# Kernel optimization log

Hardware: AMD Instinct MI355X
Metric: run time of the kernel (lower is better)

## Reference

```python
import jax, jax.numpy as jnp
import numpy as np

B, V, N, IN_F, HEADS, OUT_F = 4, 4, 1000, 64, 4, 32
D = HEADS * OUT_F  # 128, concat=True
E = 64000
NEG_SLOPE = 0.2


def setup_inputs() -> dict:
    key = jax.random.key(0)
    ks = jax.random.split(key, 8)
    x = jax.random.normal(ks[0], (B, V, N, IN_F), jnp.float32)
    edge_index = jax.random.randint(ks[1], (2, E), 0, B * N, dtype=jnp.int64)
    W = jax.random.normal(ks[2], (HEADS * OUT_F, IN_F), jnp.float32) / np.sqrt(IN_F)
    att = jax.random.normal(ks[3], (1, HEADS, 2 * OUT_F), jnp.float32) * 0.1
    in_proj_w = jax.random.normal(ks[4], (3 * D, D), jnp.float32) / np.sqrt(D)
    in_proj_b = jnp.zeros((3 * D,), jnp.float32)
    out_proj_w = jax.random.normal(ks[5], (D, D), jnp.float32) / np.sqrt(D)
    out_proj_b = jnp.zeros((D,), jnp.float32)
    bias = jnp.zeros((D,), jnp.float32)
    return dict(x=x, W=W, att=att, in_proj_w=in_proj_w, in_proj_b=in_proj_b,
                out_proj_w=out_proj_w, out_proj_b=out_proj_b, bias=bias,
                edge_index=edge_index)


def reference(x, W, att, in_proj_w, in_proj_b, out_proj_w, out_proj_b, bias, edge_index):
    Bx, Vx, Nx, _ = x.shape
    Ntot = Bx * Nx
    # intra-view GAT: shared W across views
    h = jnp.einsum('bvni,oi->bvno', x, W).reshape(Bx, Vx, Nx, HEADS, OUT_F)
    # block-diagonal placement: h_full[b*V+v, b*N:(b+1)*N] = h[b,v]
    ib = jnp.arange(Bx)
    hf = jnp.zeros((Bx, Vx, Bx, Nx, HEADS, OUT_F), x.dtype).at[ib, :, ib].set(h)
    h_full = hf.reshape(Bx * Vx, Ntot, HEADS, OUT_F)
    # add self loops
    loops = jnp.arange(Ntot, dtype=edge_index.dtype)
    src = jnp.concatenate([edge_index[0], loops])
    dst = jnp.concatenate([edge_index[1], loops])
    # attention scores (faithful to source: flatten h_full over (B*V, Ntot) and
    # index with raw node ids, i.e. gathers from block 0 only)
    h_flat = h_full.reshape(Bx * Vx * Ntot, HEADS, OUT_F)
    h_cat = jnp.concatenate([h_flat[src], h_flat[dst]], axis=-1)  # [Etot, H, 2*OUT]
    att_in = jax.nn.leaky_relu(h_cat, NEG_SLOPE)
    scores = jnp.sum(att * att_in, axis=-1)  # [Etot, HEADS]
    # per-destination segment softmax
    seg_max = jax.ops.segment_max(scores, dst, num_segments=Ntot)
    seg_max = jax.lax.stop_gradient(jnp.where(jnp.isfinite(seg_max), seg_max, 0.0))
    ex = jnp.exp(scores - seg_max[dst])
    denom = jax.ops.segment_sum(ex, dst, num_segments=Ntot)
    alpha = ex / (denom[dst] + 1e-16)  # [Etot, HEADS]
    # scatter-add aggregation, broadcast over B*V rows
    msgs = h_full[:, src] * alpha[None, :, :, None]  # [B*V, Etot, H, OUT]
    out_full = jnp.zeros_like(h_full).at[:, dst].add(msgs)
    # extract each graph's own node block
    out = out_full.reshape(Bx, Vx, Bx, Nx, HEADS, OUT_F)[ib, :, ib]  # [B,V,N,H,OUT]
    h_gat = out.reshape(Bx, Vx, Nx, HEADS * OUT_F)  # concat heads
    # inter-view mixing: MHA over the V axis per node
    seq = h_gat.transpose(0, 2, 1, 3).reshape(Bx * Nx, Vx, D)
    q, k, v = jnp.split(seq @ in_proj_w.T + in_proj_b, 3, axis=-1)
    hd = D // HEADS
    sp = lambda t: t.reshape(Bx * Nx, Vx, HEADS, hd).transpose(0, 2, 1, 3)
    q, k, v = sp(q), sp(k), sp(v)
    aw = jax.nn.softmax(jnp.einsum('bhqd,bhkd->bhqk', q, k) / jnp.sqrt(jnp.asarray(hd, x.dtype)), axis=-1)
    ao = jnp.einsum('bhqk,bhkd->bhqd', aw, v).transpose(0, 2, 1, 3).reshape(Bx * Nx, Vx, D)
    mixed = ao @ out_proj_w.T + out_proj_b
    h_mixed = mixed.reshape(Bx, Nx, Vx, D).transpose(0, 2, 1, 3)  # [B,V,N,D]
    return h_mixed + bias
```

## Files before the change

### kernel.cpp

```cpp
#include <hip/hip_runtime.h>

#define NN 1000
#define HEADS_ 4
#define DM 128
#define EE 64000
#define NTOT 4000
#define ETOT 68000
#define CAP 48
#define EB 34
#define TB 10

__device__ void gemm64_k1(float* As, float* Bs, int mi, int ni,
                          const float* __restrict__ x, const float* __restrict__ W,
                          float* __restrict__ hbuf, const float* __restrict__ att,
                          float* __restrict__ ssrc, float* __restrict__ sdst) {
  int tid = threadIdx.x;
  int m0 = mi * 64, n0 = ni * 64;
  int tx = tid & 15, ty = tid >> 4;
  const float4* A4 = (const float4*)x;
  const float4* W4 = (const float4*)W;
  float acc[4][4] = {};

  __syncthreads();
  {
    int q = tid & 15, r0 = tid >> 4;
#pragma unroll
    for (int p = 0; p < 4; ++p) {
      int r = r0 + p * 16;
      float4 v = A4[(size_t)(m0 + r) * 16 + q];
      *(float4*)&As[r * 64 + ((q ^ ((r >> 2) & 15)) << 2)] = v;
    }
#pragma unroll
    for (int p = 0; p < 4; ++p) {
      int r = r0 + p * 16;
      float4 v = W4[(size_t)(n0 + r) * 16 + q];
      *(float4*)&Bs[r * 64 + ((q ^ ((r >> 2) & 15)) << 2)] = v;
    }
  }
  __syncthreads();
#pragma unroll 4
  for (int q = 0; q < 16; ++q) {
    float4 a[4], b[4];
    int sa = (q ^ ty) << 2;
    int sb = (q ^ tx) << 2;
#pragma unroll
    for (int i = 0; i < 4; ++i)
      a[i] = *(const float4*)&As[(ty * 4 + i) * 64 + sa];
#pragma unroll
    for (int j = 0; j < 4; ++j)
      b[j] = *(const float4*)&Bs[(tx * 4 + j) * 64 + sb];
#pragma unroll
    for (int i = 0; i < 4; ++i)
#pragma unroll
      for (int j = 0; j < 4; ++j)
        acc[i][j] += a[i].x * b[j].x + a[i].y * b[j].y
                   + a[i].z * b[j].z + a[i].w * b[j].w;
  }

  int nc = n0 + tx * 4;
#pragma unroll
  for (int i = 0; i < 4; ++i) {
    int m = m0 + ty * 4 + i;
    *(float4*)&hbuf[(size_t)m * DM + nc] =
        make_float4(acc[i][0], acc[i][1], acc[i][2], acc[i][3]);
  }

  if (m0 < NN) {
    int hsel = tx >> 3;
    int h = ni * 2 + hsel;
    int kb = (tx & 7) * 4;
    float a0[4], a1[4];
#pragma unroll
    for (int j = 0; j < 4; ++j) {
      a0[j] = att[h * 64 + kb + j];
      a1[j] = att[h * 64 + 32 + kb + j];
    }
#pragma unroll
    for (int i = 0; i < 4; ++i) {
      int m = m0 + ty * 4 + i;
      float p0 = 0.f, p1 = 0.f;
#pragma unroll
      for (int j = 0; j < 4; ++j) {
        float g = acc[i][j];
        float lr = g > 0.f ? g : 0.2f * g;
        p0 += a0[j] * lr;
        p1 += a1[j] * lr;
      }
      p0 += __shfl_xor(p0, 1, 16); p1 += __shfl_xor(p1, 1, 16);
      p0 += __shfl_xor(p0, 2, 16); p1 += __shfl_xor(p1, 2, 16);
      p0 += __shfl_xor(p0, 4, 16); p1 += __shfl_xor(p1, 4, 16);
      if ((tx & 7) == 0 && m < NN) {
        ssrc[m * HEADS_ + h] = p0;
        sdst[m * HEADS_ + h] = p1;
      }
    }
  }
}

__global__ __launch_bounds__(256) void k1_kernel(const float* __restrict__ x,
                                                 const float* __restrict__ W,
                                                 const float* __restrict__ att,
                                                 float* __restrict__ hbuf,
                                                 float* __restrict__ ssrc,
                                                 float* __restrict__ sdst,
                                                 const int* __restrict__ ei,
                                                 int* __restrict__ cnt,
                                                 int* __restrict__ elist,
                                                 const float* __restrict__ inw,
                                                 const float* __restrict__ outw,
                                                 float* __restrict__ inwT,
                                                 float* __restrict__ outwT) {
  __shared__ float smem[8192];
  int bid = blockIdx.x;
  if (bid < 500) {
    gemm64_k1(smem, smem + 4096, bid >> 1, bid & 1, x, W, hbuf, att, ssrc, sdst);
  } else if (bid < 500 + EB) {
    for (int e = (bid - 500) * 256 + threadIdx.x; e < ETOT; e += EB * 256) {
      int s, d;
      if (e < EE) { s = ei[e]; d = ei[EE + e]; }
      else { s = d = e - EE; }
      int pos = atomicAdd(&cnt[d], 1);
      if (pos < CAP) elist[d * CAP + pos] = s;
    }
  } else {
    int tb = bid - (500 + EB);
    if (tb < 8) {
      for (int g = tb * 6144 + threadIdx.x; g < (tb + 1) * 6144; g += 256) {
        int col = g >> 7, k = g & 127;
        inwT[k * 384 + col] = inw[(size_t)col * 128 + k];
      }
    } else {
      int ob = tb - 8;
      for (int g = ob * 8192 + threadIdx.x; g < (ob + 1) * 8192; g += 256) {
        int col = g >> 7, k = g & 127;
        outwT[k * 128 + col] = outw[(size_t)col * 128 + k];
      }
    }
  }
}

__global__ __launch_bounds__(256) void mega2_kernel(const int* __restrict__ cnt,
                                                    const int* __restrict__ elist,
                                                    const float* __restrict__ ssrc,
                                                    const float* __restrict__ sdst,
                                                    const float* __restrict__ hbuf,
                                                    const float* __restrict__ inwT,
                                                    const float* __restrict__ inb,
                                                    const float* __restrict__ outwT,
                                                    const float* __restrict__ outb,
                                                    const float* __restrict__ bias,
                                                    float* __restrict__ out) {
  __shared__ float smem[3136];
  float* As    = smem;
  float* exsF  = smem + 2112;
  int*   srcsI = (int*)(smem + 2112 + 768);
  float* aoS   = smem;

  int tid = threadIdx.x;
  int g0n = blockIdx.x * 4;
  int kgN = (int)(blockDim.x >> 3);

  {
    int ln = tid >> 6, t64 = tid & 63;
    int d = g0n + ln;
    int m = cnt[d]; if (m > CAP) m = CAP;
    float sd = (d < NN) ? sdst[d * HEADS_ + (t64 & 3)] : 0.f;
    for (int base = 0; base < m; base += 16) {
      int i = base + (t64 >> 2);
      if (i < m) {
        int s = elist[d * CAP + i];
        if ((t64 & 3) == 0) srcsI[ln * CAP + i] = s;
        float ss = (s < NN) ? ssrc[s * HEADS_ + (t64 & 3)] : 0.f;
        exsF[ln * 192 + i * 4 + (t64 & 3)] = __expf(ss + sd);
      }
    }
  }
  __syncthreads();

  {
    int r = tid >> 4, f = tid & 15;
    int ln = r >> 2, v = r & 3;
    int d = g0n + ln, b = d / NN;
    int m = cnt[d]; if (m > CAP) m = CAP;
    int h_lo = f >> 3, h_hi = 2 + (f >> 3);
    const float* hbase = hbuf + ((size_t)(b * 4 + v) * NN) * DM + f * 4;
    float4 alo = make_float4(0.f, 0.f, 0.f, 0.f), ahi = alo;
    float dlo = 1e-16f, dhi = 1e-16f;
    int i = 0;
    for (; i + 4 <= m; i += 4) {
      float exl[4], exh[4]; unsigned sl[4]; const float* hrow[4];
#pragma unroll
      for (int u = 0; u < 4; ++u) {
        exl[u] = exsF[ln * 192 + (i + u) * 4 + h_lo];
        exh[u] = exsF[ln * 192 + (i + u) * 4 + h_hi];
        sl[u] = (unsigned)(srcsI[ln * CAP + i + u] - b * NN);
        unsigned sc = sl[u] < NN ? sl[u] : 0u;
        hrow[u] = hbase + (size_t)sc * DM;
      }
      float4 hl[4], hh[4];
#pragma unroll
      for (int u = 0; u < 4; ++u) {
        hl[u] = *(const float4*)(hrow[u]);
        hh[u] = *(const float4*)(hrow[u] + 64);
      }
#pragma unroll
      for (int u = 0; u < 4; ++u) {
        dlo += exl[u]; dhi += exh[u];
        float wl = sl[u] < NN ? exl[u] : 0.f, wh = sl[u] < NN ? exh[u] : 0.f;
        alo.x += wl * hl[u].x; alo.y += wl * hl[u].y;
        alo.z += wl * hl[u].z; alo.w += wl * hl[u].w;
        ahi.x += wh * hh[u].x; ahi.y += wh * hh[u].y;
        ahi.z += wh * hh[u].z; ahi.w += wh * hh[u].w;
      }
    }
    for (; i < m; ++i) {
      float exl = exsF[ln * 192 + i * 4 + h_lo];
      float exh = exsF[ln * 192 + i * 4 + h_hi];
      unsigned sl = (unsigned)(srcsI[ln * CAP + i] - b * NN);
      unsigned sc = sl < NN ? sl : 0u;
      const float* hrow = hbase + (size_t)sc * DM;
      float4 hl = *(const float4*)(hrow);
      float4 hh = *(const float4*)(hrow + 64);
      dlo += exl; dhi += exh;
      float wl = sl < NN ? exl : 0.f, wh = sl < NN ? exh : 0.f;
      alo.x += wl * hl.x; alo.y += wl * hl.y; alo.z += wl * hl.z; alo.w += wl * hl.w;
      ahi.x += wh * hh.x; ahi.y += wh * hh.y; ahi.z += wh * hh.z; ahi.w += wh * hh.w;
    }
    float il = 1.f / dlo, ih = 1.f / dhi;
    *(float4*)&As[r * 132 +      f * 4] = make_float4(alo.x * il, alo.y * il, alo.z * il, alo.w * il);
    *(float4*)&As[r * 132 + 64 + f * 4] = make_float4(ahi.x * ih, ahi.y * ih, ahi.z * ih, ahi.w * ih);
  }
  __syncthreads();

  int tx = tid & 63, ty = tid >> 6;
  float acc[3][4][2] = {};
  {
    const float2* BT = (const float2*)inwT;
    for (int kg = 0; kg < kgN; ++kg) {
      float4 a4[4];
#pragma unroll
      for (int i = 0; i < 4; ++i)
        a4[i] = *(const float4*)&As[(ty * 4 + i) * 132 + kg * 4];
      float2 bb[12];
#pragma unroll
      for (int kk = 0; kk < 4; ++kk)
#pragma unroll
        for (int p = 0; p < 3; ++p)
          bb[kk * 3 + p] = BT[(size_t)(kg * 4 + kk) * 192 + p * 64 + tx];
#pragma unroll
      for (int kk = 0; kk < 4; ++kk) {
        float av[4];
#pragma unroll
        for (int i = 0; i < 4; ++i)
          av[i] = kk == 0 ? a4[i].x : kk == 1 ? a4[i].y : kk == 2 ? a4[i].z : a4[i].w;
#pragma unroll
        for (int p = 0; p < 3; ++p) {
          float2 b = bb[kk * 3 + p];
#pragma unroll
          for (int i = 0; i < 4; ++i) {
            acc[p][i][0] += av[i] * b.x;
            acc[p][i][1] += av[i] * b.y;
          }
        }
      }
    }
  }

#pragma unroll
  for (int ni = 0; ni < 3; ++ni) {
    float b0 = inb[ni * 128 + tx * 2], b1 = inb[ni * 128 + tx * 2 + 1];
#pragma unroll
    for (int i = 0; i < 4; ++i) { acc[ni][i][0] += b0; acc[ni][i][1] += b1; }
  }
  float S[4][4];
#pragma unroll
  for (int vq = 0; vq < 4; ++vq)
#pragma unroll
    for (int vk = 0; vk < 4; ++vk)
      S[vq][vk] = acc[0][vq][0] * acc[1][vk][0] + acc[0][vq][1] * acc[1][vk][1];
#pragma unroll
  for (int vq = 0; vq < 4; ++vq)
#pragma unroll
    for (int vk = 0; vk < 4; ++vk) {
      float s = S[vq][vk];
      s += __shfl_xor(s, 1);
      s += __shfl_xor(s, 2);
      s += __shfl_xor(s, 4);
      s += __shfl_xor(s, 8);
      S[vq][vk] = s * 0.17677669529663687f;
    }
#pragma unroll
  for (int vq = 0; vq < 4; ++vq) {
    float mx = fmaxf(fmaxf(S[vq][0], S[vq][1]), fmaxf(S[vq][2], S[vq][3]));
    float e0 = __expf(S[vq][0] - mx), e1 = __expf(S[vq][1] - mx);
    float e2 = __expf(S[vq][2] - mx), e3 = __expf(S[vq][3] - mx);
    float inv = 1.f / (e0 + e1 + e2 + e3);
    S[vq][0] = e0 * inv; S[vq][1] = e1 * inv; S[vq][2] = e2 * inv; S[vq][3] = e3 * inv;
  }
  float ao0[4], ao1[4];
#pragma unroll
  for (int vq = 0; vq < 4; ++vq) {
    ao0[vq] = S[vq][0] * acc[2][0][0] + S[vq][1] * acc[2][1][0]
            + S[vq][2] * acc[2][2][0] + S[vq][3] * acc[2][3][0];
    ao1[vq] = S[vq][0] * acc[2][0][1] + S[vq][1] * acc[2][1][1]
            + S[vq][2] * acc[2][2][1] + S[vq][3] * acc[2][3][1];
  }
  __syncthreads();
#pragma unroll
  for (int vq = 0; vq < 4; ++vq)
    *(float2*)&aoS[(ty * 4 + vq) * 132 + tx * 2] = make_float2(ao0[vq], ao1[vq]);
  __syncthreads();

  float oc[4][2] = {};
  {
    const float2* OT = (const float2*)outwT;
    for (int kg = 0; kg < kgN; ++kg) {
      float4 a4[4];
#pragma unroll
      for (int i = 0; i < 4; ++i)
        a4[i] = *(const float4*)&aoS[(ty * 4 + i) * 132 + kg * 4];
      float2 bb[4];
#pragma unroll
      for (int kk = 0; kk < 4; ++kk)
        bb[kk] = OT[(size_t)(kg * 4 + kk) * 64 + tx];
#pragma unroll
      for (int kk = 0; kk < 4; ++kk) {
        float av[4];
#pragma unroll
        for (int i = 0; i < 4; ++i)
          av[i] = kk == 0 ? a4[i].x : kk == 1 ? a4[i].y : kk == 2 ? a4[i].z : a4[i].w;
        float2 b = bb[kk];
#pragma unroll
        for (int i = 0; i < 4; ++i) {
          oc[i][0] += av[i] * b.x;
          oc[i][1] += av[i] * b.y;
        }
      }
    }
  }

  {
    int nc = tx * 2;
    float o0 = outb[nc] + bias[nc], o1 = outb[nc + 1] + bias[nc + 1];
#pragma unroll
    for (int i = 0; i < 4; ++i) {
      int node = g0n + ty, vv = i;
      int bg = node / NN, n = node - bg * NN;
      int om = (bg * 4 + vv) * NN + n;
      *(float2*)&out[(size_t)om * DM + nc] = make_float2(oc[i][0] + o0, oc[i][1] + o1);
    }
  }
}

extern "C" void kernel_launch(void* const* d_in, const int* in_sizes, int n_in,
                              void* d_out, int out_size, void* d_ws, size_t ws_size,
                              hipStream_t stream) {
  const float* x    = (const float*)d_in[0];
  const float* W    = (const float*)d_in[1];
  const float* att  = (const float*)d_in[2];
  const float* inw  = (const float*)d_in[3];
  const float* inb  = (const float*)d_in[4];
  const float* outw = (const float*)d_in[5];
  const float* outb = (const float*)d_in[6];
  const float* bias = (const float*)d_in[7];
  const int*   ei   = (const int*)d_in[8];
  float* out = (float*)d_out;

  float* ws = (float*)d_ws;
  float* hbuf  = ws;
  float* ssrc  = ws + 12500000;
  float* sdst  = ssrc + 16000;
  int*   cnt   = (int*)(sdst + 16000);
  int*   elist = cnt + 4000;
  float* inwT  = ws + 12800000;
  float* outwT = ws + 12900000;

  hipMemsetAsync(cnt, 0, 4000 * sizeof(int), stream);

  k1_kernel<<<500 + EB + TB, 256, 0, stream>>>(x, W, att, hbuf, ssrc, sdst,
                                               ei, cnt, elist, inw, outw,
                                               inwT, outwT);
  mega2_kernel<<<NTOT / 4, 256, 0, stream>>>(cnt, elist, ssrc, sdst, hbuf,
                                             inwT, inb, outwT, outb, bias, out);
}
```

Before: 157.9 us.

## Process 8 nodes per block with split-K halves and float4 column tiles

The mega2 kernel now handles 8 nodes per 512-thread block instead of 4. In the projection GEMMs each thread covers 4 output columns using float4 weight loads, and the K dimension is split between two 32-lane halves of each wave. The halves are combined with a cross-lane shuffle. This is meant to halve the number of weight-matrix loads per node and widen the memory accesses, at the cost of more registers per thread (48 accumulators), extra shuffles, and only 500 blocks in the grid.

```diff
diff --git a/kernel.cpp b/kernel.cpp
--- a/kernel.cpp
+++ b/kernel.cpp
@@ -139,7 +139,7 @@
   }
 }
 
-__global__ __launch_bounds__(256) void mega2_kernel(const int* __restrict__ cnt,
+__global__ __launch_bounds__(512) void mega2_kernel(const int* __restrict__ cnt,
                                                     const int* __restrict__ elist,
                                                     const float* __restrict__ ssrc,
                                                     const float* __restrict__ sdst,
@@ -150,15 +150,15 @@
                                                     const float* __restrict__ outb,
                                                     const float* __restrict__ bias,
                                                     float* __restrict__ out) {
-  __shared__ float smem[3136];
+  __shared__ float smem[6528];
   float* As    = smem;
-  float* exsF  = smem + 2112;
-  int*   srcsI = (int*)(smem + 2112 + 768);
+  float* exsF  = smem + 4224;
+  int*   srcsI = (int*)(smem + 4224 + 1536);
   float* aoS   = smem;
 
   int tid = threadIdx.x;
-  int g0n = blockIdx.x * 4;
-  int kgN = (int)(blockDim.x >> 3);
+  int g0n = blockIdx.x * 8;
+  int kgH = (int)(blockDim.x >> 5);
 
   {
     int ln = tid >> 6, t64 = tid & 63;
@@ -232,21 +232,23 @@
   }
   __syncthreads();
 
-  int tx = tid & 63, ty = tid >> 6;
-  float acc[3][4][2] = {};
+  int ln = tid >> 6;
+  int kh = (tid >> 5) & 1;
+  int tx = tid & 31;
+  float acc[3][4][4] = {};
   {
-    const float2* BT = (const float2*)inwT;
-    for (int kg = 0; kg < kgN; ++kg) {
+    const float4* BT = (const float4*)inwT;
+    for (int kg = kh * kgH; kg < (kh + 1) * kgH; ++kg) {
       float4 a4[4];
 #pragma unroll
       for (int i = 0; i < 4; ++i)
-        a4[i] = *(const float4*)&As[(ty * 4 + i) * 132 + kg * 4];
-      float2 bb[12];
+        a4[i] = *(const float4*)&As[(ln * 4 + i) * 132 + kg * 4];
+      float4 bb[12];
 #pragma unroll
       for (int kk = 0; kk < 4; ++kk)
 #pragma unroll
         for (int p = 0; p < 3; ++p)
-          bb[kk * 3 + p] = BT[(size_t)(kg * 4 + kk) * 192 + p * 64 + tx];
+          bb[kk * 3 + p] = BT[(size_t)(kg * 4 + kk) * 96 + p * 32 + tx];
 #pragma unroll
       for (int kk = 0; kk < 4; ++kk) {
         float av[4];
@@ -255,29 +257,42 @@
           av[i] = kk == 0 ? a4[i].x : kk == 1 ? a4[i].y : kk == 2 ? a4[i].z : a4[i].w;
 #pragma unroll
         for (int p = 0; p < 3; ++p) {
-          float2 b = bb[kk * 3 + p];
+          float4 b = bb[kk * 3 + p];
 #pragma unroll
           for (int i = 0; i < 4; ++i) {
             acc[p][i][0] += av[i] * b.x;
             acc[p][i][1] += av[i] * b.y;
+            acc[p][i][2] += av[i] * b.z;
+            acc[p][i][3] += av[i] * b.w;
           }
         }
       }
     }
   }
+#pragma unroll
+  for (int p = 0; p < 3; ++p)
+#pragma unroll
+    for (int i = 0; i < 4; ++i)
+#pragma unroll
+      for (int j = 0; j < 4; ++j)
+        acc[p][i][j] += __shfl_xor(acc[p][i][j], 32);
 
 #pragma unroll
   for (int ni = 0; ni < 3; ++ni) {
-    float b0 = inb[ni * 128 + tx * 2], b1 = inb[ni * 128 + tx * 2 + 1];
-#pragma unroll
-    for (int i = 0; i < 4; ++i) { acc[ni][i][0] += b0; acc[ni][i][1] += b1; }
+    float4 ib = *(const float4*)&inb[ni * 128 + tx * 4];
+#pragma unroll
+    for (int i = 0; i < 4; ++i) {
+      acc[ni][i][0] += ib.x; acc[ni][i][1] += ib.y;
+      acc[ni][i][2] += ib.z; acc[ni][i][3] += ib.w;
+    }
   }
   float S[4][4];
 #pragma unroll
   for (int vq = 0; vq < 4; ++vq)
 #pragma unroll
     for (int vk = 0; vk < 4; ++vk)
-      S[vq][vk] = acc[0][vq][0] * acc[1][vk][0] + acc[0][vq][1] * acc[1][vk][1];
+      S[vq][vk] = acc[0][vq][0] * acc[1][vk][0] + acc[0][vq][1] * acc[1][vk][1]
+                + acc[0][vq][2] * acc[1][vk][2] + acc[0][vq][3] * acc[1][vk][3];
 #pragma unroll
   for (int vq = 0; vq < 4; ++vq)
 #pragma unroll
@@ -286,7 +301,6 @@
       s += __shfl_xor(s, 1);
       s += __shfl_xor(s, 2);
       s += __shfl_xor(s, 4);
-      s += __shfl_xor(s, 8);
       S[vq][vk] = s * 0.17677669529663687f;
     }
 #pragma unroll
@@ -297,57 +311,70 @@
     float inv = 1.f / (e0 + e1 + e2 + e3);
     S[vq][0] = e0 * inv; S[vq][1] = e1 * inv; S[vq][2] = e2 * inv; S[vq][3] = e3 * inv;
   }
-  float ao0[4], ao1[4];
+  float4 ao_r[4];
 #pragma unroll
   for (int vq = 0; vq < 4; ++vq) {
-    ao0[vq] = S[vq][0] * acc[2][0][0] + S[vq][1] * acc[2][1][0]
-            + S[vq][2] * acc[2][2][0] + S[vq][3] * acc[2][3][0];
-    ao1[vq] = S[vq][0] * acc[2][0][1] + S[vq][1] * acc[2][1][1]
-            + S[vq][2] * acc[2][2][1] + S[vq][3] * acc[2][3][1];
-  }
-  __syncthreads();
-#pragma unroll
-  for (int vq = 0; vq < 4; ++vq)
-    *(float2*)&aoS[(ty * 4 + vq) * 132 + tx * 2] = make_float2(ao0[vq], ao1[vq]);
-  __syncthreads();
-
-  float oc[4][2] = {};
+    ao_r[vq] = make_float4(
+        S[vq][0] * acc[2][0][0] + S[vq][1] * acc[2][1][0] + S[vq][2] * acc[2][2][0] + S[vq][3] * acc[2][3][0],
+        S[vq][0] * acc[2][0][1] + S[vq][1] * acc[2][1][1] + S[vq][2] * acc[2][2][1] + S[vq][3] * acc[2][3][1],
+        S[vq][0] * acc[2][0][2] + S[vq][1] * acc[2][1][2] + S[vq][2] * acc[2][2][2] + S[vq][3] * acc[2][3][2],
+        S[vq][0] * acc[2][0][3] + S[vq][1] * acc[2][1][3] + S[vq][2] * acc[2][2][3] + S[vq][3] * acc[2][3][3]);
+  }
+  __syncthreads();
+  if (kh == 0) {
+#pragma unroll
+    for (int vq = 0; vq < 4; ++vq)
+      *(float4*)&aoS[(ln * 4 + vq) * 132 + tx * 4] = ao_r[vq];
+  }
+  __syncthreads();
+
+  float oc[4][4] = {};
   {
-    const float2* OT = (const float2*)outwT;
-    for (int kg = 0; kg < kgN; ++kg) {
+    const float4* OT = (const float4*)outwT;
+    for (int kg = kh * kgH; kg < (kh + 1) * kgH; ++kg) {
       float4 a4[4];
 #pragma unroll
       for (int i = 0; i < 4; ++i)
-        a4[i] = *(const float4*)&aoS[(ty * 4 + i) * 132 + kg * 4];
-      float2 bb[4];
+        a4[i] = *(const float4*)&aoS[(ln * 4 + i) * 132 + kg * 4];
+      float4 bb[4];
 #pragma unroll
       for (int kk = 0; kk < 4; ++kk)
-        bb[kk] = OT[(size_t)(kg * 4 + kk) * 64 + tx];
+        bb[kk] = OT[(size_t)(kg * 4 + kk) * 32 + tx];
 #pragma unroll
       for (int kk = 0; kk < 4; ++kk) {
         float av[4];
 #pragma unroll
         for (int i = 0; i < 4; ++i)
           av[i] = kk == 0 ? a4[i].x : kk == 1 ? a4[i].y : kk == 2 ? a4[i].z : a4[i].w;
-        float2 b = bb[kk];
+        float4 b = bb[kk];
 #pragma unroll
         for (int i = 0; i < 4; ++i) {
           oc[i][0] += av[i] * b.x;
           oc[i][1] += av[i] * b.y;
+          oc[i][2] += av[i] * b.z;
+          oc[i][3] += av[i] * b.w;
         }
       }
     }
   }
-
-  {
-    int nc = tx * 2;
-    float o0 = outb[nc] + bias[nc], o1 = outb[nc + 1] + bias[nc + 1];
+#pragma unroll
+  for (int i = 0; i < 4; ++i)
+#pragma unroll
+    for (int j = 0; j < 4; ++j)
+      oc[i][j] += __shfl_xor(oc[i][j], 32);
+
+  if (kh == 0) {
+    int nc = tx * 4;
+    float4 ob = make_float4(outb[nc] + bias[nc], outb[nc + 1] + bias[nc + 1],
+                            outb[nc + 2] + bias[nc + 2], outb[nc + 3] + bias[nc + 3]);
 #pragma unroll
     for (int i = 0; i < 4; ++i) {
-      int node = g0n + ty, vv = i;
+      int node = g0n + ln, vv = i;
       int bg = node / NN, n = node - bg * NN;
       int om = (bg * 4 + vv) * NN + n;
-      *(float2*)&out[(size_t)om * DM + nc] = make_float2(oc[i][0] + o0, oc[i][1] + o1);
+      *(float4*)&out[(size_t)om * DM + nc] =
+          make_float4(oc[i][0] + ob.x, oc[i][1] + ob.y,
+                      oc[i][2] + ob.z, oc[i][3] + ob.w);
     }
   }
 }
@@ -380,6 +407,6 @@
   k1_kernel<<<500 + EB + TB, 256, 0, stream>>>(x, W, att, hbuf, ssrc, sdst,
                                                ei, cnt, elist, inw, outw,
                                                inwT, outwT);
-  mega2_kernel<<<NTOT / 4, 256, 0, stream>>>(cnt, elist, ssrc, sdst, hbuf,
+  mega2_kernel<<<NTOT / 8, 512, 0, stream>>>(cnt, elist, ssrc, sdst, hbuf,
                                              inwT, inb, outwT, outb, bias, out);
 }
```

New measurement: 154.8 us. No clear change (-1.9%).
